# Optimization experiments

Measured on AMD Instinct MI355X. Metric: run time of the kernel, lower is better.

## Reference

```python
import jax, jax.numpy as jnp
import numpy as np

N, E = 50000, 800000
NODE_DIM, EDGE_DIM, TIME_DIM, OUT_DIM, N_HEADS = 128, 64, 16, 128, 4
IN_DIM = NODE_DIM + EDGE_DIM + TIME_DIM  # msg_proj input


def setup_inputs() -> dict:
    key = jax.random.key(0)
    ks = jax.random.split(key, 8)
    x = jax.random.normal(ks[0], (N, NODE_DIM), dtype=jnp.float32)
    edge_index = jax.random.randint(ks[1], (2, E), 0, N, dtype=jnp.int32)
    edge_feat = jax.random.normal(ks[2], (E, EDGE_DIM), dtype=jnp.float32)
    time_deltas = jax.random.uniform(ks[3], (E,), dtype=jnp.float32)
    # parameters
    gammas = jnp.ones((TIME_DIM,), jnp.float32)  # ExponentialTimeDecay init_gamma=1.0
    Wm = 0.02 * jax.random.normal(ks[4], (IN_DIM, OUT_DIM), dtype=jnp.float32)
    bm = jnp.zeros((OUT_DIM,), jnp.float32)
    Wa = 0.02 * jax.random.normal(ks[5], (2 * OUT_DIM, N_HEADS), dtype=jnp.float32)
    ba = jnp.zeros((N_HEADS,), jnp.float32)
    Wo = 0.02 * jax.random.normal(ks[6], (OUT_DIM + NODE_DIM, OUT_DIM), dtype=jnp.float32)
    bo = jnp.zeros((OUT_DIM,), jnp.float32)
    ln_g = jnp.ones((OUT_DIM,), jnp.float32)
    ln_b = jnp.zeros((OUT_DIM,), jnp.float32)
    return {"x": x, "edge_index": edge_index, "edge_feat": edge_feat,
            "time_deltas": time_deltas, "gammas": gammas, "Wm": Wm, "bm": bm,
            "Wa": Wa, "ba": ba, "Wo": Wo, "bo": bo, "ln_g": ln_g, "ln_b": ln_b}


def reference(x, edge_index, edge_feat, time_deltas, gammas, Wm, bm, Wa, ba, Wo, bo, ln_g, ln_b):
    src, dst = edge_index[0], edge_index[1]
    # exponential time decay encoding: (E, TIME_DIM)
    dt = jnp.clip(time_deltas, 0.0)[:, None]
    time_enc = jnp.exp(-jax.nn.softplus(gammas)[None, :] * dt)
    # gather + project messages: (E, OUT_DIM)
    msg_in = jnp.concatenate([x[src], edge_feat, time_enc], axis=-1)
    msgs = msg_in @ Wm + bm
    # edge attention, softmax over ALL edges (dim=0, as in the torch code)
    attn_in = jnp.concatenate([msgs, x[dst]], axis=-1)  # (E, 2*OUT_DIM)
    attn_logits = attn_in @ Wa + ba                      # (E, N_HEADS)
    attn_weight = jnp.mean(jax.nn.softmax(attn_logits, axis=0), axis=-1, keepdims=True)
    weighted = msgs * attn_weight
    # scatter-add into per-node aggregates: (N, OUT_DIM)
    agg = jax.ops.segment_sum(weighted, dst, num_segments=N)
    # output MLP (dropout is identity in eval) + LayerNorm
    out = jax.nn.gelu(jnp.concatenate([agg, x], axis=-1) @ Wo + bo, approximate=False)
    mu = jnp.mean(out, axis=-1, keepdims=True)
    var = jnp.mean((out - mu) ** 2, axis=-1, keepdims=True)
    return (out - mu) / jnp.sqrt(var + 1e-5) * ln_g + ln_b
```

## Files before the change

kernel.cpp:

```cpp
#include <hip/hip_runtime.h>
#include <math.h>

#define N_NODES 50000
#define N_EDGES 800000
#define ND 128
#define ED 64
#define TD 16
#define OD 128
#define NH 4
#define INDIM 208
#define K2DIM 336
#define KPAD 352
#define WTPITCH 360
#define NPAD 50048

#define OFF_A      0ll
#define OFF_PERM   8808448ll
#define OFF_DENOM  12008448ll
#define OFF_SPG    12008464ll
#define OFF_WFUSE  12008480ll
#define OFF_BFUSE  12009312ll
#define OFF_BMO    12009328ll
#define OFF_XS4    12009456ll
#define OFF_XD4    12209456ll
#define OFF_CNT    12409456ll
#define OFF_START  12459456ll
#define OFF_CURSOR 12509472ll
#define OFF_SW     12559472ll
#define OFF_WT     12609520ll
#define OFF_EFB    12632560ll
#define OFF_XBF    38232560ll
#define WS_FLOATS  41432560ll

typedef __attribute__((ext_vector_type(8))) short short8v;
typedef __attribute__((ext_vector_type(4))) float f32x4;

__device__ inline unsigned short f2bf(float f) {
  unsigned u = __float_as_uint(f);
  unsigned r = (u + 0x7fffu + ((u >> 16) & 1u)) >> 16;
  return (unsigned short)r;
}
__device__ inline float bf2f(unsigned us) {
  return __uint_as_float(us << 16);
}

__global__ void k0_prep(const float* __restrict__ Wm, const float* __restrict__ bm,
                        const float* __restrict__ Wa, const float* __restrict__ ba,
                        const float* __restrict__ Wo, const float* __restrict__ gammas,
                        float* __restrict__ ws) {
  int b = blockIdx.x, j = threadIdx.x;
  unsigned short* Wt = (unsigned short*)(ws + OFF_WT);
  if (b < INDIM) {
    float acc = 0.f;
    for (int m = 0; m < OD; ++m) acc += Wm[b * OD + m] * Wo[m * OD + j];
    Wt[j * WTPITCH + b] = f2bf(acc);
    if (j < NH) {
      float a = 0.f;
      for (int m = 0; m < OD; ++m) a += Wm[b * OD + m] * Wa[m * NH + j];
      ws[OFF_WFUSE + (long)b * NH + j] = a;
    }
  } else if (b < K2DIM) {
    Wt[j * WTPITCH + b] = f2bf(Wo[(OD + b - INDIM) * OD + j]);
  } else {
    if (j < TD) ws[OFF_SPG + j] = log1pf(expf(gammas[j]));
    if (j < NH) {
      float a = ba[j];
      for (int m = 0; m < OD; ++m) a += bm[m] * Wa[m * NH + j];
      ws[OFF_BFUSE + j] = a;
    }
    float a2 = 0.f;
    for (int m = 0; m < OD; ++m) a2 += bm[m] * Wo[m * OD + j];
    ws[OFF_BMO + j] = a2;
    for (int p = K2DIM; p < KPAD; ++p) Wt[j * WTPITCH + p] = 0;
  }
}

__global__ __launch_bounds__(256) void k0b_nodeproj(
    const float* __restrict__ x, const float* __restrict__ Wa,
    float* __restrict__ ws) {
  __shared__ float wf[ND * NH];
  __shared__ float wab[ND * NH];
  int tid = threadIdx.x;
  for (int i = tid; i < ND * NH; i += 256) { wf[i] = ws[OFF_WFUSE + i]; wab[i] = Wa[ND * NH + i]; }
  __syncthreads();
  int lane = tid & 63, wv = tid >> 6;
  long n = (long)blockIdx.x * 4 + wv;
  if (n >= N_NODES) return;
  float v0 = x[n * ND + lane], v1 = x[n * ND + 64 + lane];
  unsigned short* xbf = (unsigned short*)(ws + OFF_XBF);
  xbf[n * ND + lane] = f2bf(v0);
  xbf[n * ND + 64 + lane] = f2bf(v1);
  float s0, s1, s2, s3, d0, d1, d2, d3;
  s0 = v0 * wf[lane * 4 + 0] + v1 * wf[(64 + lane) * 4 + 0];
  s1 = v0 * wf[lane * 4 + 1] + v1 * wf[(64 + lane) * 4 + 1];
  s2 = v0 * wf[lane * 4 + 2] + v1 * wf[(64 + lane) * 4 + 2];
  s3 = v0 * wf[lane * 4 + 3] + v1 * wf[(64 + lane) * 4 + 3];
  d0 = v0 * wab[lane * 4 + 0] + v1 * wab[(64 + lane) * 4 + 0];
  d1 = v0 * wab[lane * 4 + 1] + v1 * wab[(64 + lane) * 4 + 1];
  d2 = v0 * wab[lane * 4 + 2] + v1 * wab[(64 + lane) * 4 + 2];
  d3 = v0 * wab[lane * 4 + 3] + v1 * wab[(64 + lane) * 4 + 3];
  for (int off = 32; off; off >>= 1) {
    s0 += __shfl_xor(s0, off); s1 += __shfl_xor(s1, off);
    s2 += __shfl_xor(s2, off); s3 += __shfl_xor(s3, off);
    d0 += __shfl_xor(d0, off); d1 += __shfl_xor(d1, off);
    d2 += __shfl_xor(d2, off); d3 += __shfl_xor(d3, off);
  }
  if (lane == 0) {
    reinterpret_cast<float4*>(ws + OFF_XS4)[n] = make_float4(s0, s1, s2, s3);
    reinterpret_cast<float4*>(ws + OFF_XD4)[n] = make_float4(d0, d1, d2, d3);
  }
}

__global__ __launch_bounds__(256) void k_count(const int* __restrict__ ei,
                                               float* __restrict__ ws) {
  int* cnt = reinterpret_cast<int*>(ws + OFF_CNT);
  for (long e = (long)blockIdx.x * 256 + threadIdx.x; e < N_EDGES;
       e += (long)gridDim.x * 256)
    atomicAdd(&cnt[ei[N_EDGES + e]], 1);
}

__global__ __launch_bounds__(1024) void k_scan(float* __restrict__ ws) {
  const int* cnt = reinterpret_cast<const int*>(ws + OFF_CNT);
  int* startp = reinterpret_cast<int*>(ws + OFF_START);
  int* cursor = reinterpret_cast<int*>(ws + OFF_CURSOR);
  __shared__ int wsum[16];
  int tid = threadIdx.x;
  int lo = tid * 49, hi = min(lo + 49, N_NODES);
  int s = 0;
  for (int i = lo; i < hi; ++i) s += cnt[i];
  int lane = tid & 63, wv = tid >> 6;
  int sc = s;
  for (int off = 1; off < 64; off <<= 1) {
    int t = __shfl_up(sc, off);
    if (lane >= off) sc += t;
  }
  if (lane == 63) wsum[wv] = sc;
  __syncthreads();
  if (tid == 0) {
    int run = 0;
    for (int i = 0; i < 16; ++i) { int t = wsum[i]; wsum[i] = run; run += t; }
  }
  __syncthreads();
  int run = wsum[wv] + sc - s;
  for (int i = lo; i < hi; ++i) { startp[i] = run; cursor[i] = run; run += cnt[i]; }
  if (tid == 1023) startp[N_NODES] = run;
}

__global__ __launch_bounds__(256) void k1_logits(
    const int* __restrict__ ei, const float* __restrict__ ef,
    const float* __restrict__ td, float* __restrict__ ws) {
  __shared__ float wef[ED * NH];
  __shared__ float wte[TD * NH];
  __shared__ float bf[NH];
  __shared__ float spg[TD];
  __shared__ float part[NH];
  int tid = threadIdx.x;
  for (int i = tid; i < ED * NH; i += 256) wef[i] = ws[OFF_WFUSE + ND * NH + i];
  if (tid < TD * NH) wte[tid] = ws[OFF_WFUSE + (ND + ED) * NH + tid];
  if (tid < NH) { bf[tid] = ws[OFF_BFUSE + tid]; part[tid] = 0.f; }
  if (tid < TD) spg[tid] = ws[OFF_SPG + tid];
  __syncthreads();

  int lane = tid & 63;
  int q = lane >> 4, r = lane & 15, h = r & 3;
  long wid = ((long)blockIdx.x * 256 + tid) >> 6;
  long stride = (long)gridDim.x * 16;
  const float4* ef4 = reinterpret_cast<const float4*>(ef);
  const float* xsf = ws + OFF_XS4;
  const float* xdf = ws + OFF_XD4;
  int* cursor = reinterpret_cast<int*>(ws + OFF_CURSOR);
  uint4* perm = reinterpret_cast<uint4*>(ws + OFF_PERM);
  uint2* efb2 = reinterpret_cast<uint2*>(ws + OFF_EFB);

  float wr[16];
#pragma unroll
  for (int i = 0; i < 16; ++i) wr[i] = wef[16 * r + i];
  float spg_r = spg[r];
  float wt0 = wte[r * 4 + 0], wt1 = wte[r * 4 + 1];
  float wt2 = wte[r * 4 + 2], wt3 = wte[r * 4 + 3];
  float bfh = bf[h];
  float p = 0.f;
  int base16 = lane & 48;

  for (long e = wid * 4 + q; e < N_EDGES; e += stride) {
    int s = ei[e];
    int d = ei[N_EDGES + e];
    float dt = fmaxf(td[e], 0.f);
    float4 efv = ef4[e * 16 + r];
    float ls = xsf[4l * s + h];
    float ld = xdf[4l * d + h];
    float te = __expf(-spg_r * dt);
    uint2 eb;
    eb.x = (unsigned)f2bf(efv.x) | ((unsigned)f2bf(efv.y) << 16);
    eb.y = (unsigned)f2bf(efv.z) | ((unsigned)f2bf(efv.w) << 16);
    efb2[e * 16 + r] = eb;
    float a0 = efv.x * wr[0] + efv.y * wr[4] + efv.z * wr[8]  + efv.w * wr[12] + te * wt0;
    float a1 = efv.x * wr[1] + efv.y * wr[5] + efv.z * wr[9]  + efv.w * wr[13] + te * wt1;
    float a2 = efv.x * wr[2] + efv.y * wr[6] + efv.z * wr[10] + efv.w * wr[14] + te * wt2;
    float a3 = efv.x * wr[3] + efv.y * wr[7] + efv.z * wr[11] + efv.w * wr[15] + te * wt3;
    a0 += __shfl_xor(a0, 1); a1 += __shfl_xor(a1, 1);
    a2 += __shfl_xor(a2, 1); a3 += __shfl_xor(a3, 1);
    a0 += __shfl_xor(a0, 2); a1 += __shfl_xor(a1, 2);
    a2 += __shfl_xor(a2, 2); a3 += __shfl_xor(a3, 2);
    float v = a0;
    v = (h == 1) ? a1 : v;
    v = (h == 2) ? a2 : v;
    v = (h == 3) ? a3 : v;
    v += __shfl_xor(v, 4);
    v += __shfl_xor(v, 8);
    float ev = __expf(v + ls + ld + bfh);
    if (r < 4) p += ev;
    float e0 = __shfl(ev, base16 + 0), e1 = __shfl(ev, base16 + 1);
    float e2 = __shfl(ev, base16 + 2), e3 = __shfl(ev, base16 + 3);
    if (r == 0) {
      int pos = atomicAdd(&cursor[d], 1);
      unsigned dt16 = (unsigned)(dt * 65535.f + 0.5f);
      if (dt16 > 65535u) dt16 = 65535u;
      uint4 pk;
      pk.x = (unsigned)s | (dt16 << 16);
      pk.y = (unsigned)e;
      pk.z = (unsigned)f2bf(e0) | ((unsigned)f2bf(e1) << 16);
      pk.w = (unsigned)f2bf(e2) | ((unsigned)f2bf(e3) << 16);
      perm[pos] = pk;
    }
  }
  p += __shfl_xor(p, 16);
  p += __shfl_xor(p, 32);
  if (lane < 4) atomicAdd(&part[lane], p);
  __syncthreads();
  if (tid < NH) atomicAdd(&ws[OFF_DENOM + tid], part[tid]);
}

__global__ __launch_bounds__(256) void k4a_agg(float* __restrict__ ws) {
  __shared__ float spg_s[TD];
  __shared__ float invs[NH];
  int tid = threadIdx.x;
  if (tid < TD) spg_s[tid] = ws[OFF_SPG + tid];
  if (tid < NH) invs[tid] = 0.25f / ws[OFF_DENOM + tid];
  __syncthreads();
  int lane = tid & 63;
  long wid = (long)blockIdx.x * 4 + (tid >> 6);
  long nw = (long)gridDim.x * 4;
  const int* start = reinterpret_cast<const int*>(ws + OFF_START);
  const uint4* perm = reinterpret_cast<const uint4*>(ws + OFF_PERM);
  unsigned short* A = (unsigned short*)(ws + OFF_A);
  const unsigned short* xbf = (const unsigned short*)(ws + OFF_XBF);
  const unsigned short* efb = (const unsigned short*)(ws + OFF_EFB);
  float spg_l = spg_s[lane & 15];
  float inv0 = invs[0], inv1 = invs[1], inv2 = invs[2], inv3 = invs[3];

  for (long n = wid; n < N_NODES; n += nw) {
    int i0 = start[n], i1 = start[n + 1];
    float a0 = 0.f, a1 = 0.f, a2 = 0.f, a3 = 0.f, asw = 0.f;
    for (int base = i0; base < i1; base += 64) {
      int m = min(64, i1 - base);
      uint4 pk = make_uint4(0u, 0u, 0u, 0u);
      if (lane < m) pk = perm[base + lane];
      int j = 0;
      for (; j + 4 <= m; j += 4) {
        unsigned xu[4], eu[4], zu[4], wu[4];
#pragma unroll
        for (int u = 0; u < 4; ++u) {
          xu[u] = (unsigned)__shfl((int)pk.x, j + u);
          eu[u] = (unsigned)__shfl((int)pk.y, j + u);
          zu[u] = (unsigned)__shfl((int)pk.z, j + u);
          wu[u] = (unsigned)__shfl((int)pk.w, j + u);
        }
        unsigned xa[4], xb[4], ec[4];
#pragma unroll
        for (int u = 0; u < 4; ++u) {
          int s = (int)(xu[u] & 0xffffu);
          xa[u] = xbf[s * ND + lane];
          xb[u] = xbf[s * ND + 64 + lane];
          ec[u] = efb[(long)eu[u] * ED + lane];
        }
#pragma unroll
        for (int u = 0; u < 4; ++u) {
          float w = bf2f(zu[u] & 0xffffu) * inv0 + bf2f(zu[u] >> 16) * inv1 +
                    bf2f(wu[u] & 0xffffu) * inv2 + bf2f(wu[u] >> 16) * inv3;
          float dt = (float)(xu[u] >> 16) * (1.f / 65535.f);
          a0 += w * bf2f(xa[u]);
          a1 += w * bf2f(xb[u]);
          a2 += w * bf2f(ec[u]);
          a3 += w * __expf(-spg_l * dt);
          asw += w;
        }
      }
      for (; j < m; ++j) {
        unsigned xu = (unsigned)__shfl((int)pk.x, j);
        unsigned eu = (unsigned)__shfl((int)pk.y, j);
        unsigned zu = (unsigned)__shfl((int)pk.z, j);
        unsigned wu = (unsigned)__shfl((int)pk.w, j);
        int s = (int)(xu & 0xffffu);
        float w = bf2f(zu & 0xffffu) * inv0 + bf2f(zu >> 16) * inv1 +
                  bf2f(wu & 0xffffu) * inv2 + bf2f(wu >> 16) * inv3;
        float dt = (float)(xu >> 16) * (1.f / 65535.f);
        a0 += w * bf2f(xbf[s * ND + lane]);
        a1 += w * bf2f(xbf[s * ND + 64 + lane]);
        a2 += w * bf2f(efb[(long)eu * ED + lane]);
        a3 += w * __expf(-spg_l * dt);
        asw += w;
      }
    }
    unsigned short* Ar = A + n * KPAD;
    Ar[lane] = f2bf(a0);
    Ar[64 + lane] = f2bf(a1);
    Ar[128 + lane] = f2bf(a2);
    if (lane < TD) Ar[192 + lane] = f2bf(a3);
    Ar[INDIM + lane] = xbf[n * ND + lane];
    Ar[INDIM + 64 + lane] = xbf[n * ND + 64 + lane];
    if (lane < 16) Ar[K2DIM + lane] = 0;
    if (lane == 0) ws[OFF_SW + n] = asw;
  }
}

__global__ __launch_bounds__(256) void k4b_mlp(
    const float* __restrict__ bo, const float* __restrict__ lng,
    const float* __restrict__ lnb, const float* __restrict__ ws,
    float* __restrict__ out) {
  __shared__ unsigned short wt[128 * WTPITCH];
  __shared__ float tbl[512];
  int tid = threadIdx.x;
  {
    const unsigned* wg = (const unsigned*)(ws + OFF_WT);
    unsigned* wl = (unsigned*)wt;
    for (int i = tid; i < 128 * WTPITCH / 2; i += 256) wl[i] = wg[i];
    if (tid < 128) {
      tbl[tid] = bo[tid];
      tbl[128 + tid] = ws[OFF_BMO + tid];
      tbl[256 + tid] = lng[tid];
      tbl[384 + tid] = lnb[tid];
    }
  }
  __syncthreads();

  int lane = tid & 63, wv = tid >> 6;
  int c0 = lane & 15, grp = lane >> 4;
  long n0 = (long)blockIdx.x * 64 + (long)wv * 16;
  const unsigned short* A = (const unsigned short*)(ws + OFF_A);
  const unsigned short* Arow = A + (n0 + c0) * KPAD;

  f32x4 acc[8];
#pragma unroll
  for (int t = 0; t < 8; ++t) acc[t] = (f32x4){0.f, 0.f, 0.f, 0.f};

#pragma unroll
  for (int kt = 0; kt < 11; ++kt) {
    short8v afrag = *reinterpret_cast<const short8v*>(Arow + kt * 32 + grp * 8);
#pragma unroll
    for (int t = 0; t < 8; ++t) {
      short8v bfrag = *reinterpret_cast<const short8v*>(&wt[(t * 16 + c0) * WTPITCH + kt * 32 + grp * 8]);
      acc[t] = __builtin_amdgcn_mfma_f32_16x16x32_bf16(afrag, bfrag, acc[t], 0, 0, 0);
    }
  }

  const float* swp = ws + OFF_SW;
  float res[4][8];
#pragma unroll
  for (int r = 0; r < 4; ++r) {
    long row = n0 + grp * 4 + r;
    float sw = swp[row];
    float s = 0.f, s2 = 0.f;
#pragma unroll
    for (int t = 0; t < 8; ++t) {
      int col = c0 + 16 * t;
      float a = acc[t][r] + tbl[col] + sw * tbl[128 + col];
      float h = 0.5f * a * (1.f + erff(a * 0.70710678118654752f));
      res[r][t] = h;
      s += h; s2 += h * h;
    }
    s += __shfl_xor(s, 1);  s2 += __shfl_xor(s2, 1);
    s += __shfl_xor(s, 2);  s2 += __shfl_xor(s2, 2);
    s += __shfl_xor(s, 4);  s2 += __shfl_xor(s2, 4);
    s += __shfl_xor(s, 8);  s2 += __shfl_xor(s2, 8);
    float mu = s * (1.f / 128.f);
    float var = s2 * (1.f / 128.f) - mu * mu;
    float rstd = rsqrtf(var + 1e-5f);
    if (row < N_NODES) {
      float* op = out + row * OD;
#pragma unroll
      for (int t = 0; t < 8; ++t) {
        int col = c0 + 16 * t;
        op[col] = (res[r][t] - mu) * rstd * tbl[256 + col] + tbl[384 + col];
      }
    }
  }
}

extern "C" void kernel_launch(void* const* d_in, const int* in_sizes, int n_in,
                              void* d_out, int out_size, void* d_ws, size_t ws_size,
                              hipStream_t stream) {
  const float* x   = (const float*)d_in[0];
  const int*   ei  = (const int*)d_in[1];
  const float* ef  = (const float*)d_in[2];
  const float* td  = (const float*)d_in[3];
  const float* gm  = (const float*)d_in[4];
  const float* Wm  = (const float*)d_in[5];
  const float* bm  = (const float*)d_in[6];
  const float* Wa  = (const float*)d_in[7];
  const float* ba  = (const float*)d_in[8];
  const float* Wo  = (const float*)d_in[9];
  const float* bo  = (const float*)d_in[10];
  const float* lng = (const float*)d_in[11];
  const float* lnb = (const float*)d_in[12];
  float* ws = (float*)d_ws;
  float* out = (float*)d_out;
  if (ws_size < (size_t)WS_FLOATS * 4) return;

  hipMemsetAsync(ws + OFF_CNT, 0, 50000 * 4, stream);
  hipMemsetAsync(ws + OFF_DENOM, 0, 64, stream);

  k0_prep<<<K2DIM + 1, 128, 0, stream>>>(Wm, bm, Wa, ba, Wo, gm, ws);
  k0b_nodeproj<<<12500, 256, 0, stream>>>(x, Wa, ws);
  k_count<<<2048, 256, 0, stream>>>(ei, ws);
  k_scan<<<1, 1024, 0, stream>>>(ws);
  k1_logits<<<2048, 256, 0, stream>>>(ei, ef, td, ws);
  k4a_agg<<<2048, 256, 0, stream>>>(ws);
  k4b_mlp<<<(NPAD / 64), 256, 0, stream>>>(bo, lng, lnb, ws, out);
}
```

Before: 480.3 us.

## Split edge logits kernel into edge-feature projection and per-edge scatter kernels

```diff
diff --git a/kernel.cpp b/kernel.cpp
--- a/kernel.cpp
+++ b/kernel.cpp
@@ -16,21 +16,22 @@
 
 #define OFF_A      0ll
 #define OFF_PERM   8808448ll
-#define OFF_DENOM  12008448ll
-#define OFF_SPG    12008464ll
-#define OFF_WFUSE  12008480ll
-#define OFF_BFUSE  12009312ll
-#define OFF_BMO    12009328ll
-#define OFF_XS4    12009456ll
-#define OFF_XD4    12209456ll
-#define OFF_CNT    12409456ll
-#define OFF_START  12459456ll
-#define OFF_CURSOR 12509472ll
-#define OFF_SW     12559472ll
-#define OFF_WT     12609520ll
-#define OFF_EFB    12632560ll
-#define OFF_XBF    38232560ll
-#define WS_FLOATS  41432560ll
+#define OFF_EFP4   12008448ll
+#define OFF_DENOM  15208448ll
+#define OFF_SPG    15208464ll
+#define OFF_WFUSE  15208480ll
+#define OFF_BFUSE  15209312ll
+#define OFF_BMO    15209328ll
+#define OFF_XS4    15209456ll
+#define OFF_XD4    15409456ll
+#define OFF_CNT    15609456ll
+#define OFF_START  15659456ll
+#define OFF_CURSOR 15709472ll
+#define OFF_SW     15759472ll
+#define OFF_WT     15809520ll
+#define OFF_EFB    15832560ll
+#define OFF_XBF    41432560ll
+#define WS_FLOATS  44632560ll
 
 typedef __attribute__((ext_vector_type(8))) short short8v;
 typedef __attribute__((ext_vector_type(4))) float f32x4;
@@ -146,58 +147,34 @@
   if (tid == 1023) startp[N_NODES] = run;
 }
 
-__global__ __launch_bounds__(256) void k1_logits(
-    const int* __restrict__ ei, const float* __restrict__ ef,
-    const float* __restrict__ td, float* __restrict__ ws) {
+__global__ __launch_bounds__(256) void k_ef(const float* __restrict__ ef,
+                                            float* __restrict__ ws) {
   __shared__ float wef[ED * NH];
-  __shared__ float wte[TD * NH];
-  __shared__ float bf[NH];
-  __shared__ float spg[TD];
-  __shared__ float part[NH];
   int tid = threadIdx.x;
   for (int i = tid; i < ED * NH; i += 256) wef[i] = ws[OFF_WFUSE + ND * NH + i];
-  if (tid < TD * NH) wte[tid] = ws[OFF_WFUSE + (ND + ED) * NH + tid];
-  if (tid < NH) { bf[tid] = ws[OFF_BFUSE + tid]; part[tid] = 0.f; }
-  if (tid < TD) spg[tid] = ws[OFF_SPG + tid];
-  __syncthreads();
-
+  __syncthreads();
   int lane = tid & 63;
   int q = lane >> 4, r = lane & 15, h = r & 3;
   long wid = ((long)blockIdx.x * 256 + tid) >> 6;
   long stride = (long)gridDim.x * 16;
   const float4* ef4 = reinterpret_cast<const float4*>(ef);
-  const float* xsf = ws + OFF_XS4;
-  const float* xdf = ws + OFF_XD4;
-  int* cursor = reinterpret_cast<int*>(ws + OFF_CURSOR);
-  uint4* perm = reinterpret_cast<uint4*>(ws + OFF_PERM);
   uint2* efb2 = reinterpret_cast<uint2*>(ws + OFF_EFB);
+  float* efp = ws + OFF_EFP4;
 
   float wr[16];
 #pragma unroll
   for (int i = 0; i < 16; ++i) wr[i] = wef[16 * r + i];
-  float spg_r = spg[r];
-  float wt0 = wte[r * 4 + 0], wt1 = wte[r * 4 + 1];
-  float wt2 = wte[r * 4 + 2], wt3 = wte[r * 4 + 3];
-  float bfh = bf[h];
-  float p = 0.f;
-  int base16 = lane & 48;
 
   for (long e = wid * 4 + q; e < N_EDGES; e += stride) {
-    int s = ei[e];
-    int d = ei[N_EDGES + e];
-    float dt = fmaxf(td[e], 0.f);
     float4 efv = ef4[e * 16 + r];
-    float ls = xsf[4l * s + h];
-    float ld = xdf[4l * d + h];
-    float te = __expf(-spg_r * dt);
     uint2 eb;
     eb.x = (unsigned)f2bf(efv.x) | ((unsigned)f2bf(efv.y) << 16);
     eb.y = (unsigned)f2bf(efv.z) | ((unsigned)f2bf(efv.w) << 16);
     efb2[e * 16 + r] = eb;
-    float a0 = efv.x * wr[0] + efv.y * wr[4] + efv.z * wr[8]  + efv.w * wr[12] + te * wt0;
-    float a1 = efv.x * wr[1] + efv.y * wr[5] + efv.z * wr[9]  + efv.w * wr[13] + te * wt1;
-    float a2 = efv.x * wr[2] + efv.y * wr[6] + efv.z * wr[10] + efv.w * wr[14] + te * wt2;
-    float a3 = efv.x * wr[3] + efv.y * wr[7] + efv.z * wr[11] + efv.w * wr[15] + te * wt3;
+    float a0 = efv.x * wr[0] + efv.y * wr[4] + efv.z * wr[8]  + efv.w * wr[12];
+    float a1 = efv.x * wr[1] + efv.y * wr[5] + efv.z * wr[9]  + efv.w * wr[13];
+    float a2 = efv.x * wr[2] + efv.y * wr[6] + efv.z * wr[10] + efv.w * wr[14];
+    float a3 = efv.x * wr[3] + efv.y * wr[7] + efv.z * wr[11] + efv.w * wr[15];
     a0 += __shfl_xor(a0, 1); a1 += __shfl_xor(a1, 1);
     a2 += __shfl_xor(a2, 1); a3 += __shfl_xor(a3, 1);
     a0 += __shfl_xor(a0, 2); a1 += __shfl_xor(a1, 2);
@@ -208,25 +185,64 @@
     v = (h == 3) ? a3 : v;
     v += __shfl_xor(v, 4);
     v += __shfl_xor(v, 8);
-    float ev = __expf(v + ls + ld + bfh);
-    if (r < 4) p += ev;
-    float e0 = __shfl(ev, base16 + 0), e1 = __shfl(ev, base16 + 1);
-    float e2 = __shfl(ev, base16 + 2), e3 = __shfl(ev, base16 + 3);
-    if (r == 0) {
-      int pos = atomicAdd(&cursor[d], 1);
-      unsigned dt16 = (unsigned)(dt * 65535.f + 0.5f);
-      if (dt16 > 65535u) dt16 = 65535u;
-      uint4 pk;
-      pk.x = (unsigned)s | (dt16 << 16);
-      pk.y = (unsigned)e;
-      pk.z = (unsigned)f2bf(e0) | ((unsigned)f2bf(e1) << 16);
-      pk.w = (unsigned)f2bf(e2) | ((unsigned)f2bf(e3) << 16);
-      perm[pos] = pk;
-    }
-  }
-  p += __shfl_xor(p, 16);
-  p += __shfl_xor(p, 32);
-  if (lane < 4) atomicAdd(&part[lane], p);
+    if (r < 4) efp[e * 4 + r] = v;
+  }
+}
+
+__global__ __launch_bounds__(256) void k1s(const int* __restrict__ ei,
+                                           const float* __restrict__ td,
+                                           float* __restrict__ ws) {
+  __shared__ float spg[TD];
+  __shared__ float wteL[TD * NH];
+  __shared__ float bfL[NH];
+  __shared__ float part[NH];
+  int tid = threadIdx.x;
+  if (tid < TD) spg[tid] = ws[OFF_SPG + tid];
+  if (tid < TD * NH) wteL[tid] = ws[OFF_WFUSE + (ND + ED) * NH + tid];
+  if (tid < NH) { bfL[tid] = ws[OFF_BFUSE + tid]; part[tid] = 0.f; }
+  __syncthreads();
+
+  int* cursor = reinterpret_cast<int*>(ws + OFF_CURSOR);
+  uint4* perm = reinterpret_cast<uint4*>(ws + OFF_PERM);
+  long e = (long)blockIdx.x * 256 + tid;
+  float p0 = 0.f, p1 = 0.f, p2 = 0.f, p3 = 0.f;
+  if (e < N_EDGES) {
+    int s = ei[e], d = ei[N_EDGES + e];
+    float dt = fmaxf(td[e], 0.f);
+    float4 ep = reinterpret_cast<const float4*>(ws + OFF_EFP4)[e];
+    float4 xs = reinterpret_cast<const float4*>(ws + OFF_XS4)[s];
+    float4 xd = reinterpret_cast<const float4*>(ws + OFF_XD4)[d];
+    float l0 = ep.x + xs.x + xd.x + bfL[0];
+    float l1 = ep.y + xs.y + xd.y + bfL[1];
+    float l2 = ep.z + xs.z + xd.z + bfL[2];
+    float l3 = ep.w + xs.w + xd.w + bfL[3];
+#pragma unroll
+    for (int k = 0; k < TD; ++k) {
+      float te = __expf(-spg[k] * dt);
+      l0 += te * wteL[k * 4 + 0];
+      l1 += te * wteL[k * 4 + 1];
+      l2 += te * wteL[k * 4 + 2];
+      l3 += te * wteL[k * 4 + 3];
+    }
+    p0 = __expf(l0); p1 = __expf(l1); p2 = __expf(l2); p3 = __expf(l3);
+    unsigned dt16 = (unsigned)(dt * 65535.f + 0.5f);
+    if (dt16 > 65535u) dt16 = 65535u;
+    int pos = atomicAdd(&cursor[d], 1);
+    uint4 pk;
+    pk.x = (unsigned)s | (dt16 << 16);
+    pk.y = (unsigned)e;
+    pk.z = (unsigned)f2bf(p0) | ((unsigned)f2bf(p1) << 16);
+    pk.w = (unsigned)f2bf(p2) | ((unsigned)f2bf(p3) << 16);
+    perm[pos] = pk;
+  }
+  for (int off = 32; off; off >>= 1) {
+    p0 += __shfl_xor(p0, off); p1 += __shfl_xor(p1, off);
+    p2 += __shfl_xor(p2, off); p3 += __shfl_xor(p3, off);
+  }
+  if ((tid & 63) == 0) {
+    atomicAdd(&part[0], p0); atomicAdd(&part[1], p1);
+    atomicAdd(&part[2], p2); atomicAdd(&part[3], p3);
+  }
   __syncthreads();
   if (tid < NH) atomicAdd(&ws[OFF_DENOM + tid], part[tid]);
 }
@@ -270,8 +286,8 @@
 #pragma unroll
         for (int u = 0; u < 4; ++u) {
           int s = (int)(xu[u] & 0xffffu);
-          xa[u] = xbf[s * ND + lane];
-          xb[u] = xbf[s * ND + 64 + lane];
+          xa[u] = xbf[(long)s * ND + lane];
+          xb[u] = xbf[(long)s * ND + 64 + lane];
           ec[u] = efb[(long)eu[u] * ED + lane];
         }
 #pragma unroll
@@ -295,8 +311,8 @@
         float w = bf2f(zu & 0xffffu) * inv0 + bf2f(zu >> 16) * inv1 +
                   bf2f(wu & 0xffffu) * inv2 + bf2f(wu >> 16) * inv3;
         float dt = (float)(xu >> 16) * (1.f / 65535.f);
-        a0 += w * bf2f(xbf[s * ND + lane]);
-        a1 += w * bf2f(xbf[s * ND + 64 + lane]);
+        a0 += w * bf2f(xbf[(long)s * ND + lane]);
+        a1 += w * bf2f(xbf[(long)s * ND + 64 + lane]);
         a2 += w * bf2f(efb[(long)eu * ED + lane]);
         a3 += w * __expf(-spg_l * dt);
         asw += w;
@@ -414,7 +430,8 @@
   k0b_nodeproj<<<12500, 256, 0, stream>>>(x, Wa, ws);
   k_count<<<2048, 256, 0, stream>>>(ei, ws);
   k_scan<<<1, 1024, 0, stream>>>(ws);
-  k1_logits<<<2048, 256, 0, stream>>>(ei, ef, td, ws);
+  k_ef<<<4096, 256, 0, stream>>>(ef, ws);
+  k1s<<<(N_EDGES + 255) / 256, 256, 0, stream>>>(ei, td, ws);
   k4a_agg<<<2048, 256, 0, stream>>>(ws);
   k4b_mlp<<<(NPAD / 64), 256, 0, stream>>>(bo, lng, lnb, ws, out);
 }
```

New measurement: 494.2 us. +2.9%, slower.

## Replace cursor-atomic scatter with rank-based CSR fill and edge-indexed info

Applied to the files above, without the earlier changes.

```diff
diff --git a/kernel.cpp b/kernel.cpp
--- a/kernel.cpp
+++ b/kernel.cpp
@@ -15,22 +15,23 @@
 #define NPAD 50048
 
 #define OFF_A      0ll
-#define OFF_PERM   8808448ll
-#define OFF_DENOM  12008448ll
-#define OFF_SPG    12008464ll
-#define OFF_WFUSE  12008480ll
-#define OFF_BFUSE  12009312ll
-#define OFF_BMO    12009328ll
-#define OFF_XS4    12009456ll
-#define OFF_XD4    12209456ll
-#define OFF_CNT    12409456ll
-#define OFF_START  12459456ll
-#define OFF_CURSOR 12509472ll
-#define OFF_SW     12559472ll
-#define OFF_WT     12609520ll
-#define OFF_EFB    12632560ll
-#define OFF_XBF    38232560ll
-#define WS_FLOATS  41432560ll
+#define OFF_EINFO  8808448ll
+#define OFF_PERM32 12008448ll
+#define OFF_RANK   12808448ll
+#define OFF_DENOM  13608448ll
+#define OFF_SPG    13608464ll
+#define OFF_WFUSE  13608480ll
+#define OFF_BFUSE  13609312ll
+#define OFF_BMO    13609328ll
+#define OFF_XS4    13609456ll
+#define OFF_XD4    13809456ll
+#define OFF_CNT    14009456ll
+#define OFF_START  14059456ll
+#define OFF_SW     14109472ll
+#define OFF_WT     14159520ll
+#define OFF_EFB    14182560ll
+#define OFF_XBF    39782560ll
+#define WS_FLOATS  42982560ll
 
 typedef __attribute__((ext_vector_type(8))) short short8v;
 typedef __attribute__((ext_vector_type(4))) float f32x4;
@@ -114,15 +115,15 @@
 __global__ __launch_bounds__(256) void k_count(const int* __restrict__ ei,
                                                float* __restrict__ ws) {
   int* cnt = reinterpret_cast<int*>(ws + OFF_CNT);
+  int* rank = reinterpret_cast<int*>(ws + OFF_RANK);
   for (long e = (long)blockIdx.x * 256 + threadIdx.x; e < N_EDGES;
        e += (long)gridDim.x * 256)
-    atomicAdd(&cnt[ei[N_EDGES + e]], 1);
+    rank[e] = atomicAdd(&cnt[ei[N_EDGES + e]], 1);
 }
 
 __global__ __launch_bounds__(1024) void k_scan(float* __restrict__ ws) {
   const int* cnt = reinterpret_cast<const int*>(ws + OFF_CNT);
   int* startp = reinterpret_cast<int*>(ws + OFF_START);
-  int* cursor = reinterpret_cast<int*>(ws + OFF_CURSOR);
   __shared__ int wsum[16];
   int tid = threadIdx.x;
   int lo = tid * 49, hi = min(lo + 49, N_NODES);
@@ -142,11 +143,23 @@
   }
   __syncthreads();
   int run = wsum[wv] + sc - s;
-  for (int i = lo; i < hi; ++i) { startp[i] = run; cursor[i] = run; run += cnt[i]; }
+  for (int i = lo; i < hi; ++i) { startp[i] = run; run += cnt[i]; }
   if (tid == 1023) startp[N_NODES] = run;
 }
 
-__global__ __launch_bounds__(256) void k1_logits(
+__global__ __launch_bounds__(256) void k_fill4(const int* __restrict__ ei,
+                                               float* __restrict__ ws) {
+  const int* startp = reinterpret_cast<const int*>(ws + OFF_START);
+  const int* rank = reinterpret_cast<const int*>(ws + OFF_RANK);
+  int* perm32 = reinterpret_cast<int*>(ws + OFF_PERM32);
+  for (long e = (long)blockIdx.x * 256 + threadIdx.x; e < N_EDGES;
+       e += (long)gridDim.x * 256) {
+    int d = ei[N_EDGES + e];
+    perm32[startp[d] + rank[e]] = (int)e;
+  }
+}
+
+__global__ __launch_bounds__(256) void k1f(
     const int* __restrict__ ei, const float* __restrict__ ef,
     const float* __restrict__ td, float* __restrict__ ws) {
   __shared__ float wef[ED * NH];
@@ -168,9 +181,8 @@
   const float4* ef4 = reinterpret_cast<const float4*>(ef);
   const float* xsf = ws + OFF_XS4;
   const float* xdf = ws + OFF_XD4;
-  int* cursor = reinterpret_cast<int*>(ws + OFF_CURSOR);
-  uint4* perm = reinterpret_cast<uint4*>(ws + OFF_PERM);
   uint2* efb2 = reinterpret_cast<uint2*>(ws + OFF_EFB);
+  uint4* einfo4 = reinterpret_cast<uint4*>(ws + OFF_EINFO);
 
   float wr[16];
 #pragma unroll
@@ -213,15 +225,14 @@
     float e0 = __shfl(ev, base16 + 0), e1 = __shfl(ev, base16 + 1);
     float e2 = __shfl(ev, base16 + 2), e3 = __shfl(ev, base16 + 3);
     if (r == 0) {
-      int pos = atomicAdd(&cursor[d], 1);
       unsigned dt16 = (unsigned)(dt * 65535.f + 0.5f);
       if (dt16 > 65535u) dt16 = 65535u;
       uint4 pk;
       pk.x = (unsigned)s | (dt16 << 16);
-      pk.y = (unsigned)e;
-      pk.z = (unsigned)f2bf(e0) | ((unsigned)f2bf(e1) << 16);
-      pk.w = (unsigned)f2bf(e2) | ((unsigned)f2bf(e3) << 16);
-      perm[pos] = pk;
+      pk.y = (unsigned)f2bf(e0) | ((unsigned)f2bf(e1) << 16);
+      pk.z = (unsigned)f2bf(e2) | ((unsigned)f2bf(e3) << 16);
+      pk.w = 0u;
+      einfo4[e] = pk;
     }
   }
   p += __shfl_xor(p, 16);
@@ -242,7 +253,8 @@
   long wid = (long)blockIdx.x * 4 + (tid >> 6);
   long nw = (long)gridDim.x * 4;
   const int* start = reinterpret_cast<const int*>(ws + OFF_START);
-  const uint4* perm = reinterpret_cast<const uint4*>(ws + OFF_PERM);
+  const int* perm32 = reinterpret_cast<const int*>(ws + OFF_PERM32);
+  const uint4* einfo4 = reinterpret_cast<const uint4*>(ws + OFF_EINFO);
   unsigned short* A = (unsigned short*)(ws + OFF_A);
   const unsigned short* xbf = (const unsigned short*)(ws + OFF_XBF);
   const unsigned short* efb = (const unsigned short*)(ws + OFF_EFB);
@@ -254,24 +266,25 @@
     float a0 = 0.f, a1 = 0.f, a2 = 0.f, a3 = 0.f, asw = 0.f;
     for (int base = i0; base < i1; base += 64) {
       int m = min(64, i1 - base);
-      uint4 pk = make_uint4(0u, 0u, 0u, 0u);
-      if (lane < m) pk = perm[base + lane];
+      int eidx = 0;
+      if (lane < m) eidx = perm32[base + lane];
+      uint4 pk = einfo4[eidx];
       int j = 0;
       for (; j + 4 <= m; j += 4) {
         unsigned xu[4], eu[4], zu[4], wu[4];
 #pragma unroll
         for (int u = 0; u < 4; ++u) {
           xu[u] = (unsigned)__shfl((int)pk.x, j + u);
-          eu[u] = (unsigned)__shfl((int)pk.y, j + u);
-          zu[u] = (unsigned)__shfl((int)pk.z, j + u);
-          wu[u] = (unsigned)__shfl((int)pk.w, j + u);
+          eu[u] = (unsigned)__shfl(eidx, j + u);
+          zu[u] = (unsigned)__shfl((int)pk.y, j + u);
+          wu[u] = (unsigned)__shfl((int)pk.z, j + u);
         }
         unsigned xa[4], xb[4], ec[4];
 #pragma unroll
         for (int u = 0; u < 4; ++u) {
           int s = (int)(xu[u] & 0xffffu);
-          xa[u] = xbf[s * ND + lane];
-          xb[u] = xbf[s * ND + 64 + lane];
+          xa[u] = xbf[(long)s * ND + lane];
+          xb[u] = xbf[(long)s * ND + 64 + lane];
           ec[u] = efb[(long)eu[u] * ED + lane];
         }
 #pragma unroll
@@ -288,15 +301,15 @@
       }
       for (; j < m; ++j) {
         unsigned xu = (unsigned)__shfl((int)pk.x, j);
-        unsigned eu = (unsigned)__shfl((int)pk.y, j);
-        unsigned zu = (unsigned)__shfl((int)pk.z, j);
-        unsigned wu = (unsigned)__shfl((int)pk.w, j);
+        unsigned eu = (unsigned)__shfl(eidx, j);
+        unsigned zu = (unsigned)__shfl((int)pk.y, j);
+        unsigned wu = (unsigned)__shfl((int)pk.z, j);
         int s = (int)(xu & 0xffffu);
         float w = bf2f(zu & 0xffffu) * inv0 + bf2f(zu >> 16) * inv1 +
                   bf2f(wu & 0xffffu) * inv2 + bf2f(wu >> 16) * inv3;
         float dt = (float)(xu >> 16) * (1.f / 65535.f);
-        a0 += w * bf2f(xbf[s * ND + lane]);
-        a1 += w * bf2f(xbf[s * ND + 64 + lane]);
+        a0 += w * bf2f(xbf[(long)s * ND + lane]);
+        a1 += w * bf2f(xbf[(long)s * ND + 64 + lane]);
         a2 += w * bf2f(efb[(long)eu * ED + lane]);
         a3 += w * __expf(-spg_l * dt);
         asw += w;
@@ -414,7 +427,8 @@
   k0b_nodeproj<<<12500, 256, 0, stream>>>(x, Wa, ws);
   k_count<<<2048, 256, 0, stream>>>(ei, ws);
   k_scan<<<1, 1024, 0, stream>>>(ws);
-  k1_logits<<<2048, 256, 0, stream>>>(ei, ef, td, ws);
+  k_fill4<<<2048, 256, 0, stream>>>(ei, ws);
+  k1f<<<2048, 256, 0, stream>>>(ei, ef, td, ws);
   k4a_agg<<<2048, 256, 0, stream>>>(ws);
   k4b_mlp<<<(NPAD / 64), 256, 0, stream>>>(bo, lng, lnb, ws, out);
 }
```

After: 421.4 us. 1.14x faster.
